# Optimization experiments

Hardware: AMD Instinct MI355X
Metric: run time of the kernel (lower is better)

The kernel has to match this reference:

```python
import jax, jax.numpy as jnp
import numpy as np

N, E, B = 65536, 131072, 2048
NUM_FEATURES, EDGE_FEATURES, DIM = 75, 16, 64


def setup_inputs() -> dict:
    key = jax.random.key(0)
    ks = jax.random.split(key, 24)

    def p(i, shape, scale=0.05):
        return jax.random.normal(ks[i], shape, dtype=jnp.float32) * scale

    return {
        "node_features": p(0, (N, NUM_FEATURES), 1.0),
        "edge_features": p(1, (E, EDGE_FEATURES), 1.0),
        "edge_index": jax.random.randint(ks[2], (2, E), 0, N),
        "graph_index": jnp.sort(jax.random.randint(ks[3], (N,), 0, B)),
        "lin0_w": p(4, (NUM_FEATURES, DIM)),
        "lin0_b": p(5, (DIM,)),
        "mlp_w1": p(6, (EDGE_FEATURES, 128)),
        "mlp_b1": p(7, (128,)),
        "mlp_w2": p(8, (128, DIM * DIM)),
        "mlp_b2": p(9, (DIM * DIM,)),
        "conv_bias": p(10, (DIM,)),
        "gru_w_ih": p(11, (3 * DIM, DIM)),
        "gru_w_hh": p(12, (3 * DIM, DIM)),
        "gru_b_ih": p(13, (3 * DIM,)),
        "gru_b_hh": p(14, (3 * DIM,)),
        "lstm_w_ih": p(15, (4 * DIM, 2 * DIM)),
        "lstm_w_hh": p(16, (4 * DIM, DIM)),
        "lstm_b_ih": p(17, (4 * DIM,)),
        "lstm_b_hh": p(18, (4 * DIM,)),
    }


def reference(node_features, edge_features, edge_index, graph_index,
              lin0_w, lin0_b, mlp_w1, mlp_b1, mlp_w2, mlp_b2, conv_bias,
              gru_w_ih, gru_w_hh, gru_b_ih, gru_b_hh,
              lstm_w_ih, lstm_w_hh, lstm_b_ih, lstm_b_hh):
    n = node_features.shape[0]
    d = DIM
    src, dst = edge_index[0], edge_index[1]

    # edge-conditioned weights (identical every iteration in the original loop)
    ew = jnp.maximum(edge_features @ mlp_w1 + mlp_b1, 0.0) @ mlp_w2 + mlp_b2
    W = ew.reshape(-1, d, d)  # [E, d, d]
    counts = jnp.maximum(
        jax.ops.segment_sum(jnp.ones(src.shape[0], jnp.float32), dst, num_segments=n), 1.0)

    out = jnp.maximum(node_features @ lin0_w + lin0_b, 0.0)
    h = out
    for _ in range(3):
        # NNConv: gather src, per-edge matmul, scatter-mean to dst
        msg = jnp.einsum('ed,edf->ef', out[src], W)
        agg = jax.ops.segment_sum(msg, dst, num_segments=n) / counts[:, None]
        m = jnp.maximum(agg + conv_bias, 0.0)
        # GRU step (seq len 1)
        gi = m @ gru_w_ih.T + gru_b_ih
        gh = h @ gru_w_hh.T + gru_b_hh
        r = jax.nn.sigmoid(gi[:, :d] + gh[:, :d])
        z = jax.nn.sigmoid(gi[:, d:2 * d] + gh[:, d:2 * d])
        nn_ = jnp.tanh(gi[:, 2 * d:] + r * gh[:, 2 * d:])
        h = (1.0 - z) * nn_ + z * h
        out = h
    feat_map = out

    # Set2Set pooling, 3 processing steps
    q_star = jnp.zeros((B, 2 * d), jnp.float32)
    hs = jnp.zeros((B, d), jnp.float32)
    cs = jnp.zeros((B, d), jnp.float32)
    for _ in range(3):
        gates = q_star @ lstm_w_ih.T + lstm_b_ih + hs @ lstm_w_hh.T + lstm_b_hh
        i_g = jax.nn.sigmoid(gates[:, :d])
        f_g = jax.nn.sigmoid(gates[:, d:2 * d])
        g_g = jnp.tanh(gates[:, 2 * d:3 * d])
        o_g = jax.nn.sigmoid(gates[:, 3 * d:])
        cs = f_g * cs + i_g * g_g
        hs = o_g * jnp.tanh(cs)
        q = hs  # [B, d]
        e = jnp.sum(out * q[graph_index], axis=-1)  # [N]
        e = e - jax.ops.segment_max(e, graph_index, num_segments=B)[graph_index]
        a = jnp.exp(e)
        a = a / (jax.ops.segment_sum(a, graph_index, num_segments=B)[graph_index] + 1e-16)
        rvec = jax.ops.segment_sum(a[:, None] * out, graph_index, num_segments=B)
        q_star = jnp.concatenate([q, rvec], axis=-1)
    return (q_star, feat_map)
```

## Files before the change

kernel.cpp:

```cpp
#include <hip/hip_runtime.h>
#include <hip/hip_bf16.h>

#define GN 65536
#define GE 131072
#define GB 2048

typedef __attribute__((ext_vector_type(8))) short short8;
typedef __attribute__((ext_vector_type(4))) float floatx4;

static __device__ __forceinline__ float sigm(float x) { return 1.0f / (1.0f + __expf(-x)); }
static __device__ __forceinline__ float bf2f(unsigned short u) {
    union { unsigned int i; float f; } v; v.i = ((unsigned int)u) << 16; return v.f;
}
static __device__ __forceinline__ int geti(const void* p, long long i, int f64) {
    return f64 ? (int)((const long long*)p)[i] : ((const int*)p)[i];
}

struct DetectArgs { const void* src[17]; int nhalf[17]; int fi[17]; };
__global__ void k_detect(DetectArgs a, const unsigned int* __restrict__ pe,
                         const unsigned int* __restrict__ pg,
                         int* __restrict__ flags, int* __restrict__ flagE,
                         int* __restrict__ flagG) {
    __shared__ unsigned int sA[256], sB[256];
    if (blockIdx.x >= 17) {
        const unsigned int* p = (blockIdx.x == 17) ? pe : pg;
        const long long nwords = (blockIdx.x == 17) ? (long long)2 * GE : (long long)GN;
        const long long lim = nwords < 16384 ? nwords : 16384;
        unsigned int acc = 0;
        for (long long w = 1 + 2 * (long long)threadIdx.x; w < lim; w += 512) acc |= p[w];
        sA[threadIdx.x] = acc;
        __syncthreads();
        for (int st = 128; st > 0; st >>= 1) {
            if (threadIdx.x < st) sA[threadIdx.x] |= sA[threadIdx.x + st];
            __syncthreads();
        }
        if (threadIdx.x == 0) *((blockIdx.x == 17) ? flagE : flagG) = (sA[0] == 0u) ? 1 : 0;
        return;
    }
    const unsigned short* p = (const unsigned short*)a.src[blockIdx.x];
    const int n0 = a.nhalf[blockIdx.x];
    const int n = n0 < 16384 ? n0 : 16384;
    unsigned int any = 0, orEven = 0;
    for (int i = threadIdx.x; i < n; i += 256) {
        const unsigned short u = p[i];
        const float av = fabsf(bf2f(u));
        if (!(av <= 1e6f)) any = 1u;
        if ((i & 1) == 0) orEven |= u;
    }
    sA[threadIdx.x] = any; sB[threadIdx.x] = orEven;
    __syncthreads();
    for (int s = 128; s > 0; s >>= 1) {
        if (threadIdx.x < s) {
            sA[threadIdx.x] |= sA[threadIdx.x + s];
            sB[threadIdx.x] |= sB[threadIdx.x + s];
        }
        __syncthreads();
    }
    if (threadIdx.x == 0) flags[a.fi[blockIdx.x]] = (sA[0] || sB[0] == 0u) ? 1 : 0;
}

struct CvtArgs { const void* src[15]; float* dst[15]; int n[15]; int fi[15]; int pre[16]; };
__global__ void k_cvt_all(CvtArgs a, const int* __restrict__ flags) {
    const int b = blockIdx.x;
    int t = 0;
    while (t < 14 && b >= a.pre[t + 1]) ++t;
    const int i = (b - a.pre[t]) * 256 + threadIdx.x;
    if (i >= a.n[t]) return;
    const int f = flags[a.fi[t]];
    a.dst[t][i] = f ? ((const float*)a.src[t])[i] : bf2f(((const unsigned short*)a.src[t])[i]);
}

__global__ __launch_bounds__(256) void k_t2(const void* __restrict__ src,
                                            __hip_bfloat16* __restrict__ w2P,
                                            const int* __restrict__ flag) {
    const int tid8 = blockIdx.x * 256 + threadIdx.x;
    const int quad = tid8 & 3, lr = (tid8 >> 2) & 15, rb = (tid8 >> 6) & 7,
              kk = (tid8 >> 9) & 3, t = tid8 >> 11;
    const int n = t * 128 + rb * 16 + lr;
    const int k0 = kk * 32 + quad * 8;
    const int isf32 = *flag;
    short8 v;
    #pragma unroll
    for (int j = 0; j < 8; ++j) {
        const size_t si = (size_t)(k0 + j) * 4096 + n;
        const float f = isf32 ? ((const float*)src)[si] : bf2f(((const unsigned short*)src)[si]);
        const __hip_bfloat16 b = __float2bfloat16(f);
        v[j] = *(const short*)&b;
    }
    *(short8*)(w2P + (size_t)tid8 * 8) = v;
}

__global__ void k_gpack2(const float* __restrict__ w_ih, const float* __restrict__ w_hh,
                         __hip_bfloat16* __restrict__ gwp) {
    const int t = blockIdx.x * 256 + threadIdx.x;
    if (t >= 3072) return;
    const int lane = t & 63;
    const int kk = (t >> 6) & 1;
    const int nb = (t >> 7) % 12;
    const int mat = t / 1536;
    const float* W = mat ? w_hh : w_ih;
    const int c = nb * 16 + (lane & 15);
    const int k0 = kk * 32 + (lane >> 4) * 8;
    short8 hi, lo;
    #pragma unroll
    for (int j = 0; j < 8; ++j) {
        const float v = W[c * 64 + k0 + j];
        const __hip_bfloat16 bh = __float2bfloat16(v);
        hi[j] = *(const short*)&bh;
        const __hip_bfloat16 bl = __float2bfloat16(v - __bfloat162float(bh));
        lo[j] = *(const short*)&bl;
    }
    const size_t base = (size_t)(((mat * 12 + nb) * 2 + kk) * 2);
    *(short8*)(gwp + (base + 0) * 512 + lane * 8) = hi;
    *(short8*)(gwp + (base + 1) * 512 + lane * 8) = lo;
}

__global__ void k_counts(const void* __restrict__ eidx, const int* __restrict__ fi64,
                         float* __restrict__ counts, int E_) {
    int e = blockIdx.x * 256 + threadIdx.x;
    if (e < E_) atomicAdd(&counts[geti(eidx, (long long)E_ + e, *fi64)], 1.0f);
}

__global__ void k_rowptr(const void* __restrict__ gi, const int* __restrict__ fi64,
                         int* __restrict__ rowptr, int N_, int B_) {
    int g = blockIdx.x * 256 + threadIdx.x;
    if (g > B_) return;
    const int f64 = *fi64;
    int lo = 0, hi = N_;
    while (lo < hi) { int mid = (lo + hi) >> 1; if (geti(gi, mid, f64) < g) lo = mid + 1; else hi = mid; }
    rowptr[g] = lo;
}

__global__ __launch_bounds__(256) void k_lin0(const void* __restrict__ nf_raw,
                                              const float* __restrict__ w,
                                              const float* __restrict__ b,
                                              float* __restrict__ out,
                                              const int* __restrict__ flag) {
    const int ln = threadIdx.x >> 6;
    const int d = threadIdx.x & 63;
    const int n = blockIdx.x * 4 + ln;
    const int isf32 = *flag;
    __shared__ float s_nf[4][76];
    const size_t base = (size_t)n * 75;
    s_nf[ln][d] = isf32 ? ((const float*)nf_raw)[base + d] : bf2f(((const unsigned short*)nf_raw)[base + d]);
    if (d < 11) s_nf[ln][64 + d] = isf32 ? ((const float*)nf_raw)[base + 64 + d]
                                         : bf2f(((const unsigned short*)nf_raw)[base + 64 + d]);
    __syncthreads();
    float acc = b[d];
    #pragma unroll
    for (int i = 0; i < 75; ++i) acc += s_nf[ln][i] * w[i * 64 + d];
    out[(size_t)n * 64 + d] = fmaxf(acc, 0.0f);
}

__global__ __launch_bounds__(256) void k1_h1(const void* __restrict__ ef_raw,
                                             const float* __restrict__ w1,
                                             const float* __restrict__ b1,
                                             __hip_bfloat16* __restrict__ h1,
                                             const int* __restrict__ flag) {
    const int le = threadIdx.x >> 7;
    const int j = threadIdx.x & 127;
    const int e = blockIdx.x * 2 + le;
    const int isf32 = *flag;
    __shared__ float efs[2][16];
    if (j < 16) {
        const size_t idx = (size_t)e * 16 + j;
        efs[le][j] = isf32 ? ((const float*)ef_raw)[idx] : bf2f(((const unsigned short*)ef_raw)[idx]);
    }
    __syncthreads();
    float acc = b1[j];
    #pragma unroll
    for (int i = 0; i < 16; ++i) acc += efs[le][i] * w1[i * 128 + j];
    h1[(size_t)e * 128 + j] = __float2bfloat16(fmaxf(acc, 0.0f));
}

__global__ __launch_bounds__(512) void k23_fused(const __hip_bfloat16* __restrict__ h1,
                                                 const __hip_bfloat16* __restrict__ w2P,
                                                 const float* __restrict__ b2,
                                                 const float* __restrict__ out,
                                                 const void* __restrict__ eidx,
                                                 const int* __restrict__ fi64,
                                                 float* __restrict__ agg) {
    __shared__ __align__(16) __hip_bfloat16 As[128 * 128];
    __shared__ float yT[64][65];
    const int tid = threadIdx.x;
    const int e0 = blockIdx.x * 128;
    const int f64 = *fi64;

    const int wave = tid >> 6, lane = tid & 63;
    const int wm = (wave >> 2) * 64;
    const int wn = (wave & 3) * 32;
    const int lr = lane & 15, quad = lane >> 4;

    {
        const int r = tid >> 2;
        const int cb = (tid & 3) * 32;
        #pragma unroll
        for (int j = 0; j < 4; ++j) {
            const int c = cb + j * 8;
            short8 v = *(const short8*)(h1 + (size_t)(e0 + r) * 128 + c);
            const int byte = (r * 256 + c * 2) ^ ((r & 7) << 4);
            *(short8*)((char*)As + byte) = v;
        }
    }
    __shared__ float yT2[64][129];
    {
        const int e = tid >> 2, d0 = (tid & 3) * 16;
        const int s = geti(eidx, e0 + e, f64);
        const float* srow = out + (size_t)s * 64 + d0;
        #pragma unroll
        for (int j = 0; j < 4; ++j) {
            float4 v = *(const float4*)(srow + j * 4);
            yT2[d0 + j * 4 + 0][e] = v.x;
            yT2[d0 + j * 4 + 1][e] = v.y;
            yT2[d0 + j * 4 + 2][e] = v.z;
            yT2[d0 + j * 4 + 3][e] = v.w;
        }
    }
    __syncthreads();

    const int lin = (lr * 4 + quad) * 8;
    const int sxa = (lr & 7) << 4;
    float msum[4][2][4] = {};

#define K23_LOADB(dst, tt)                                                      \
    _Pragma("unroll")                                                           \
    for (int kk = 0; kk < 4; ++kk) {                                            \
        _Pragma("unroll")                                                       \
        for (int nt = 0; nt < 2; ++nt) {                                        \
            const int g = ((tt) * 4 + kk) * 8 + (wn >> 4) + nt;                 \
            dst[kk][nt] = *(const short8*)(w2P + (size_t)g * 512 + lin);        \
        }                                                                       \
    }                                                                           \
    __builtin_amdgcn_sched_barrier(0);

#define K23_BODY(tt, buf) {                                                     \
    const int n0 = (tt) * 128;                                                  \
    const int dcur = (n0 + wn) >> 6;                                            \
    const float b2v0 = b2[n0 + wn + lr];                                        \
    const float b2v1 = b2[n0 + wn + 16 + lr];                                   \
    floatx4 acc[4][2] = {};                                                     \
    _Pragma("unroll")                                                           \
    for (int kk = 0; kk < 4; ++kk) {                                            \
        short8 a0, a1, a2, a3;                                                  \
        {                                                                       \
            const int cb = kk * 64 + quad * 16;                                 \
            a0 = *(const short8*)((const char*)As + (((wm + 0 * 16 + lr) * 256 + cb) ^ sxa)); \
            a1 = *(const short8*)((const char*)As + (((wm + 1 * 16 + lr) * 256 + cb) ^ sxa)); \
            a2 = *(const short8*)((const char*)As + (((wm + 2 * 16 + lr) * 256 + cb) ^ sxa)); \
            a3 = *(const short8*)((const char*)As + (((wm + 3 * 16 + lr) * 256 + cb) ^ sxa)); \
        }                                                                       \
        __builtin_amdgcn_s_setprio(1);                                          \
        acc[0][0] = __builtin_amdgcn_mfma_f32_16x16x32_bf16(a0, buf[kk][0], acc[0][0], 0, 0, 0); \
        acc[0][1] = __builtin_amdgcn_mfma_f32_16x16x32_bf16(a0, buf[kk][1], acc[0][1], 0, 0, 0); \
        acc[1][0] = __builtin_amdgcn_mfma_f32_16x16x32_bf16(a1, buf[kk][0], acc[1][0], 0, 0, 0); \
        acc[1][1] = __builtin_amdgcn_mfma_f32_16x16x32_bf16(a1, buf[kk][1], acc[1][1], 0, 0, 0); \
        acc[2][0] = __builtin_amdgcn_mfma_f32_16x16x32_bf16(a2, buf[kk][0], acc[2][0], 0, 0, 0); \
        acc[2][1] = __builtin_amdgcn_mfma_f32_16x16x32_bf16(a2, buf[kk][1], acc[2][1], 0, 0, 0); \
        acc[3][0] = __builtin_amdgcn_mfma_f32_16x16x32_bf16(a3, buf[kk][0], acc[3][0], 0, 0, 0); \
        acc[3][1] = __builtin_amdgcn_mfma_f32_16x16x32_bf16(a3, buf[kk][1], acc[3][1], 0, 0, 0); \
        __builtin_amdgcn_s_setprio(0);                                          \
    }                                                                           \
    _Pragma("unroll")                                                           \
    for (int mt = 0; mt < 4; ++mt) {                                            \
        _Pragma("unroll")                                                       \
        for (int r = 0; r < 4; ++r) {                                           \
            const float yv = yT2[dcur][wm + mt * 16 + quad * 4 + r];            \
            msum[mt][0][r] = fmaf(yv, acc[mt][0][r] + b2v0, msum[mt][0][r]);    \
            msum[mt][1][r] = fmaf(yv, acc[mt][1][r] + b2v1, msum[mt][1][r]);    \
        }                                                                       \
    }                                                                           \
}

    short8 bA[4][2], bB[4][2];
    K23_LOADB(bA, 0)
    #pragma unroll 1
    for (int t = 0; t < 32; t += 2) {
        K23_LOADB(bB, t + 1)
        K23_BODY(t, bA)
        if (t + 2 < 32) { K23_LOADB(bA, t + 2) }
        K23_BODY(t + 1, bB)
    }
#undef K23_LOADB
#undef K23_BODY

    const int fbase = (wn & 32);
    #pragma unroll
    for (int mt = 0; mt < 4; ++mt)
        #pragma unroll
        for (int r = 0; r < 4; ++r) {
            const int row = wm + mt * 16 + quad * 4 + r;
            const int dn = geti(eidx, (long long)GE + e0 + row, f64);
            #pragma unroll
            for (int nt = 0; nt < 2; ++nt)
                atomicAdd(&agg[(size_t)dn * 64 + fbase + nt * 16 + lr], msum[mt][nt][r]);
        }
}

__global__ __launch_bounds__(256) void k4_gru(const float* __restrict__ agg,
                                              const float* __restrict__ counts,
                                              const float* __restrict__ cbias,
                                              const __hip_bfloat16* __restrict__ gwp,
                                              const float* __restrict__ b_ih,
                                              const float* __restrict__ b_hh,
                                              float* __restrict__ out) {
    const int wv = threadIdx.x >> 6, lane = threadIdx.x & 63;
    const int lr = lane & 15, quad = lane >> 4;
    const int wnb0 = blockIdx.x * 64 + wv * 16;
    const int node = wnb0 + lr;

    const float rcnt = 1.0f / fmaxf(counts[node], 1.0f);
    const float* ap = agg + (size_t)node * 64;
    const float* hp = out + (size_t)node * 64;
    short8 am[2], ah[2];
    #pragma unroll
    for (int kk = 0; kk < 2; ++kk) {
        const int k0 = kk * 32 + quad * 8;
        #pragma unroll
        for (int j = 0; j < 8; ++j) {
            const float mv = fmaxf(ap[k0 + j] * rcnt + cbias[k0 + j], 0.0f);
            const __hip_bfloat16 mb = __float2bfloat16(mv);
            am[kk][j] = *(const short*)&mb;
            const __hip_bfloat16 hb = __float2bfloat16(hp[k0 + j]);
            ah[kk][j] = *(const short*)&hb;
        }
    }

    floatx4 ai[12] = {}, ahh[12] = {};
    #pragma unroll
    for (int nb = 0; nb < 12; ++nb) {
        #pragma unroll
        for (int kk = 0; kk < 2; ++kk) {
            #pragma unroll
            for (int part = 0; part < 2; ++part) {
                const short8 bi = *(const short8*)(gwp + (size_t)(((0 * 12 + nb) * 2 + kk) * 2 + part) * 512 + lane * 8);
                ai[nb] = __builtin_amdgcn_mfma_f32_16x16x32_bf16(am[kk], bi, ai[nb], 0, 0, 0);
                const short8 bh = *(const short8*)(gwp + (size_t)(((1 * 12 + nb) * 2 + kk) * 2 + part) * 512 + lane * 8);
                ahh[nb] = __builtin_amdgcn_mfma_f32_16x16x32_bf16(ah[kk], bh, ahh[nb], 0, 0, 0);
            }
        }
    }

    #pragma unroll
    for (int f = 0; f < 4; ++f) {
        const int d = f * 16 + lr;
        const float bir = b_ih[d],       bhr = b_hh[d];
        const float biz = b_ih[64 + d],  bhz = b_hh[64 + d];
        const float bin = b_ih[128 + d], bhn = b_hh[128 + d];
        #pragma unroll
        for (int r = 0; r < 4; ++r) {
            const int row = wnb0 + quad * 4 + r;
            const float rr = sigm(ai[f][r] + bir + ahh[f][r] + bhr);
            const float zz = sigm(ai[f + 4][r] + biz + ahh[f + 4][r] + bhz);
            const float nn = tanhf(ai[f + 8][r] + bin + rr * (ahh[f + 8][r] + bhn));
            const float hd = out[(size_t)row * 64 + d];
            out[(size_t)row * 64 + d] = (1.0f - zz) * nn + zz * hd;
        }
    }
}

__global__ __launch_bounds__(256) void k5_fused(float* __restrict__ qstar,
                                                const float* __restrict__ w_ih,
                                                const float* __restrict__ w_hh,
                                                const float* __restrict__ b_ih,
                                                const float* __restrict__ b_hh,
                                                const float* __restrict__ out,
                                                const int* __restrict__ rowptr) {
    const int g = blockIdx.x;
    const int j = threadIdx.x;
    __shared__ float qs[128], hv[64], gates[256];
    __shared__ float smw[4], sSw[4], srw[4][64];
    if (j < 128) qs[j] = 0.0f;
    if (j < 64) hv[j] = 0.0f;
    float creg = 0.0f;
    const int wv = j >> 6, lane = j & 63;
    const int start = rowptr[g], end = rowptr[g + 1];
    const float bsum = b_ih[j] + b_hh[j];

    for (int step = 0; step < 3; ++step) {
        __syncthreads();
        float acc = bsum;
        for (int k4 = 0; k4 < 128; k4 += 4) {
            float4 v = *(const float4*)(w_ih + (size_t)j * 128 + k4);
            const float* pv = (const float*)&v;
            #pragma unroll
            for (int t = 0; t < 4; ++t) acc += qs[k4 + t] * pv[t];
        }
        for (int k4 = 0; k4 < 64; k4 += 4) {
            float4 v = *(const float4*)(w_hh + (size_t)j * 64 + k4);
            const float* pv = (const float*)&v;
            #pragma unroll
            for (int t = 0; t < 4; ++t) acc += hv[k4 + t] * pv[t];
        }
        gates[j] = acc;
        __syncthreads();
        if (j < 64) {
            const float ig = sigm(gates[j]);
            const float fg = sigm(gates[64 + j]);
            const float gg = tanhf(gates[128 + j]);
            const float og = sigm(gates[192 + j]);
            creg = fg * creg + ig * gg;
            const float h = og * tanhf(creg);
            hv[j] = h;
            qs[j] = h;
        }
        __syncthreads();
        const float q = hv[lane];
        float m = -3.4e38f, S = 0.0f, racc = 0.0f;
        for (int n = start + wv; n < end; n += 4) {
            const float ov = out[(size_t)n * 64 + lane];
            float p = ov * q;
            #pragma unroll
            for (int off = 1; off < 64; off <<= 1) p += __shfl_xor(p, off);
            if (p > m) {
                const float sc = __expf(m - p);
                S = S * sc + 1.0f;
                racc = racc * sc + ov;
                m = p;
            } else {
                const float w = __expf(p - m);
                S += w;
                racc += w * ov;
            }
        }
        if (lane == 0) { smw[wv] = m; sSw[wv] = S; }
        srw[wv][lane] = racc;
        __syncthreads();
        if (wv == 0) {
            const float mstar = fmaxf(fmaxf(smw[0], smw[1]), fmaxf(smw[2], smw[3]));
            float Ssum = 0.0f, rsum = 0.0f;
            #pragma unroll
            for (int i = 0; i < 4; ++i) {
                const float sc = __expf(smw[i] - mstar);
                Ssum += sSw[i] * sc;
                rsum += srw[i][lane] * sc;
            }
            qs[64 + lane] = rsum / (Ssum + 1e-16f);
        }
    }
    __syncthreads();
    if (j < 128) qstar[(size_t)g * 128 + j] = qs[j];
}

__global__ void k_out(const float* __restrict__ qstar, const float* __restrict__ outb,
                      float* __restrict__ dst, int nq, int nfeat, int out_n) {
    int i = blockIdx.x * 256 + threadIdx.x;
    if (i >= out_n) return;
    float v = 0.0f;
    if (i < nq) v = qstar[i];
    else if (i - nq < nfeat) v = outb[i - nq];
    dst[i] = v;
}

extern "C" void kernel_launch(void* const* d_in, const int* in_sizes, int n_in,
                              void* d_out, int out_size, void* d_ws, size_t ws_size,
                              hipStream_t stream) {
    constexpr int N = GN, E = GE, B = GB;

    char* ws = (char*)d_ws;
    size_t off = 0;
    auto alloc = [&](size_t bytes) { size_t o = off; off = (off + bytes + 255) & ~(size_t)255; return o; };

    int*   fl     = (int*)  (ws + alloc(19 * 4));
    int*   flagE  = (int*)  (ws + alloc(256));
    int*   flagG  = (int*)  (ws + alloc(256));
    float* counts = (float*)(ws + alloc((size_t)N * 4));
    int*   rowptr = (int*)  (ws + alloc((size_t)(B + 1) * 4));
    float* outbuf = (float*)(ws + alloc((size_t)N * 64 * 4));
    float* agg    = (float*)(ws + alloc((size_t)N * 64 * 4));
    float* qstar  = (float*)(ws + alloc((size_t)B * 128 * 4));
    __hip_bfloat16* h1  = (__hip_bfloat16*)(ws + alloc((size_t)E * 128 * 2));
    __hip_bfloat16* w2P = (__hip_bfloat16*)(ws + alloc((size_t)4096 * 128 * 2));
    __hip_bfloat16* gwp = (__hip_bfloat16*)(ws + alloc((size_t)2 * 12 * 2 * 2 * 512 * 2));

    const int fidx[15]  = {4, 5, 6, 7, 8, 9, 10, 11, 12, 13, 14, 15, 16, 17, 18};
    const int fsize[15] = {75 * 64, 64, 16 * 128, 128, 128 * 4096, 4096, 64,
                           192 * 64, 192 * 64, 192, 192, 256 * 128, 256 * 64, 256, 256};
    float* F[19] = {};
    for (int t = 0; t < 15; ++t) F[fidx[t]] = (float*)(ws + alloc((size_t)fsize[t] * 4));

    DetectArgs da;
    da.src[0] = d_in[0]; da.nhalf[0] = N * 75; da.fi[0] = 0;
    da.src[1] = d_in[1]; da.nhalf[1] = E * 16; da.fi[1] = 1;
    for (int t = 0; t < 15; ++t) { da.src[2 + t] = d_in[fidx[t]]; da.nhalf[2 + t] = fsize[t]; da.fi[2 + t] = fidx[t]; }
    k_detect<<<19, 256, 0, stream>>>(da, (const unsigned int*)d_in[2],
                                     (const unsigned int*)d_in[3], fl, flagE, flagG);

    CvtArgs ca;
    int pre = 0;
    for (int t = 0; t < 15; ++t) {
        ca.src[t] = d_in[fidx[t]]; ca.dst[t] = F[fidx[t]]; ca.n[t] = fsize[t]; ca.fi[t] = fidx[t];
        ca.pre[t] = pre; pre += (fsize[t] + 255) / 256;
    }
    ca.pre[15] = pre;
    k_cvt_all<<<pre, 256, 0, stream>>>(ca, fl);
    k_t2<<<256, 256, 0, stream>>>(d_in[8], w2P, fl + 8);
    k_gpack2<<<12, 256, 0, stream>>>(F[11], F[12], gwp);

    hipMemsetAsync(counts, 0, (size_t)N * 4, stream);
    hipMemsetAsync(qstar, 0, (size_t)B * 128 * 4, stream);

    k_counts<<<E / 256, 256, 0, stream>>>(d_in[2], flagE, counts, E);
    k_rowptr<<<(B + 1 + 255) / 256, 256, 0, stream>>>(d_in[3], flagG, rowptr, N, B);
    k_lin0<<<N / 4, 256, 0, stream>>>(d_in[0], F[4], F[5], outbuf, fl + 0);
    k1_h1<<<E / 2, 256, 0, stream>>>(d_in[1], F[6], F[7], h1, fl + 1);

    for (int it = 0; it < 3; ++it) {
        hipMemsetAsync(agg, 0, (size_t)N * 64 * 4, stream);
        k23_fused<<<E / 128, 512, 0, stream>>>(h1, w2P, F[9], outbuf, d_in[2], flagE, agg);
        k4_gru<<<N / 64, 256, 0, stream>>>(agg, counts, F[10], gwp, F[13], F[14], outbuf);
    }
    k5_fused<<<B, 256, 0, stream>>>(qstar, F[15], F[16], F[17], F[18], outbuf, rowptr);
    k_out<<<(out_size + 255) / 256, 256, 0, stream>>>(qstar, outbuf, (float*)d_out,
                                                      B * 128, N * 64, out_size);
}
```

Measured before the change: 1.053 ms.

## Shrink edge tile to 64 and reduce partial messages in LDS before atomics

The fused edge-weight/message kernel now handles 64 edges per 256-thread block instead of 128 edges per 512 threads. All four waves share the same A rows and split the output columns. Waves whose column slices map to the same feature half first sum their partials in shared memory. The block then issues one coalesced atomicAdd per (edge, feature), using destination indices cached in LDS. This halves global atomic traffic and lowers LDS use so more blocks can be resident, but each block now re-reads the full w2 weight matrix for half as many edges and adds extra barriers.

```diff
diff --git a/kernel.cpp b/kernel.cpp
--- a/kernel.cpp
+++ b/kernel.cpp
@@ -173,24 +173,25 @@
     h1[(size_t)e * 128 + j] = __float2bfloat16(fmaxf(acc, 0.0f));
 }
 
-__global__ __launch_bounds__(512) void k23_fused(const __hip_bfloat16* __restrict__ h1,
+__global__ __launch_bounds__(256) void k23_fused(const __hip_bfloat16* __restrict__ h1,
                                                  const __hip_bfloat16* __restrict__ w2P,
                                                  const float* __restrict__ b2,
                                                  const float* __restrict__ out,
                                                  const void* __restrict__ eidx,
                                                  const int* __restrict__ fi64,
                                                  float* __restrict__ agg) {
-    __shared__ __align__(16) __hip_bfloat16 As[128 * 128];
+    __shared__ __align__(16) __hip_bfloat16 As[64 * 128];
     __shared__ float yT[64][65];
+    __shared__ int sdx[64];
     const int tid = threadIdx.x;
-    const int e0 = blockIdx.x * 128;
+    const int e0 = blockIdx.x * 64;
     const int f64 = *fi64;
 
     const int wave = tid >> 6, lane = tid & 63;
-    const int wm = (wave >> 2) * 64;
-    const int wn = (wave & 3) * 32;
+    const int wn = wave * 32;
     const int lr = lane & 15, quad = lane >> 4;
 
+    if (tid < 64) sdx[tid] = geti(eidx, (long long)GE + e0 + tid, f64);
     {
         const int r = tid >> 2;
         const int cb = (tid & 3) * 32;
@@ -202,7 +203,6 @@
             *(short8*)((char*)As + byte) = v;
         }
     }
-    __shared__ float yT2[64][129];
     {
         const int e = tid >> 2, d0 = (tid & 3) * 16;
         const int s = geti(eidx, e0 + e, f64);
@@ -210,10 +210,10 @@
         #pragma unroll
         for (int j = 0; j < 4; ++j) {
             float4 v = *(const float4*)(srow + j * 4);
-            yT2[d0 + j * 4 + 0][e] = v.x;
-            yT2[d0 + j * 4 + 1][e] = v.y;
-            yT2[d0 + j * 4 + 2][e] = v.z;
-            yT2[d0 + j * 4 + 3][e] = v.w;
+            yT[d0 + j * 4 + 0][e] = v.x;
+            yT[d0 + j * 4 + 1][e] = v.y;
+            yT[d0 + j * 4 + 2][e] = v.z;
+            yT[d0 + j * 4 + 3][e] = v.w;
         }
     }
     __syncthreads();
@@ -244,10 +244,10 @@
         short8 a0, a1, a2, a3;                                                  \
         {                                                                       \
             const int cb = kk * 64 + quad * 16;                                 \
-            a0 = *(const short8*)((const char*)As + (((wm + 0 * 16 + lr) * 256 + cb) ^ sxa)); \
-            a1 = *(const short8*)((const char*)As + (((wm + 1 * 16 + lr) * 256 + cb) ^ sxa)); \
-            a2 = *(const short8*)((const char*)As + (((wm + 2 * 16 + lr) * 256 + cb) ^ sxa)); \
-            a3 = *(const short8*)((const char*)As + (((wm + 3 * 16 + lr) * 256 + cb) ^ sxa)); \
+            a0 = *(const short8*)((const char*)As + (((0 * 16 + lr) * 256 + cb) ^ sxa)); \
+            a1 = *(const short8*)((const char*)As + (((1 * 16 + lr) * 256 + cb) ^ sxa)); \
+            a2 = *(const short8*)((const char*)As + (((2 * 16 + lr) * 256 + cb) ^ sxa)); \
+            a3 = *(const short8*)((const char*)As + (((3 * 16 + lr) * 256 + cb) ^ sxa)); \
         }                                                                       \
         __builtin_amdgcn_s_setprio(1);                                          \
         acc[0][0] = __builtin_amdgcn_mfma_f32_16x16x32_bf16(a0, buf[kk][0], acc[0][0], 0, 0, 0); \
@@ -264,7 +264,7 @@
     for (int mt = 0; mt < 4; ++mt) {                                            \
         _Pragma("unroll")                                                       \
         for (int r = 0; r < 4; ++r) {                                           \
-            const float yv = yT2[dcur][wm + mt * 16 + quad * 4 + r];            \
+            const float yv = yT[dcur][mt * 16 + quad * 4 + r];                  \
             msum[mt][0][r] = fmaf(yv, acc[mt][0][r] + b2v0, msum[mt][0][r]);    \
             msum[mt][1][r] = fmaf(yv, acc[mt][1][r] + b2v1, msum[mt][1][r]);    \
         }                                                                       \
@@ -283,17 +283,35 @@
 #undef K23_LOADB
 #undef K23_BODY
 
-    const int fbase = (wn & 32);
-    #pragma unroll
-    for (int mt = 0; mt < 4; ++mt)
-        #pragma unroll
-        for (int r = 0; r < 4; ++r) {
-            const int row = wm + mt * 16 + quad * 4 + r;
-            const int dn = geti(eidx, (long long)GE + e0 + row, f64);
-            #pragma unroll
-            for (int nt = 0; nt < 2; ++nt)
-                atomicAdd(&agg[(size_t)dn * 64 + fbase + nt * 16 + lr], msum[mt][nt][r]);
-        }
+    __syncthreads();
+    float* mg = (float*)As;
+    const int fb = (wn & 32);
+    if (wave < 2) {
+        #pragma unroll
+        for (int mt = 0; mt < 4; ++mt)
+            #pragma unroll
+            for (int r = 0; r < 4; ++r)
+                #pragma unroll
+                for (int nt = 0; nt < 2; ++nt)
+                    mg[(mt * 16 + quad * 4 + r) * 64 + fb + nt * 16 + lr] = msum[mt][nt][r];
+    }
+    __syncthreads();
+    if (wave >= 2) {
+        #pragma unroll
+        for (int mt = 0; mt < 4; ++mt)
+            #pragma unroll
+            for (int r = 0; r < 4; ++r)
+                #pragma unroll
+                for (int nt = 0; nt < 2; ++nt)
+                    mg[(mt * 16 + quad * 4 + r) * 64 + fb + nt * 16 + lr] += msum[mt][nt][r];
+    }
+    __syncthreads();
+    #pragma unroll
+    for (int i = 0; i < 16; ++i) {
+        const int o = i * 256 + tid;
+        const int row = o >> 6, col = o & 63;
+        atomicAdd(&agg[(size_t)sdx[row] * 64 + col], mg[o]);
+    }
 }
 
 __global__ __launch_bounds__(256) void k4_gru(const float* __restrict__ agg,
@@ -506,7 +524,7 @@
 
     for (int it = 0; it < 3; ++it) {
         hipMemsetAsync(agg, 0, (size_t)N * 64 * 4, stream);
-        k23_fused<<<E / 128, 512, 0, stream>>>(h1, w2P, F[9], outbuf, d_in[2], flagE, agg);
+        k23_fused<<<E / 64, 256, 0, stream>>>(h1, w2P, F[9], outbuf, d_in[2], flagE, agg);
         k4_gru<<<N / 64, 256, 0, stream>>>(agg, counts, F[10], gwp, F[13], F[14], outbuf);
     }
     k5_fused<<<B, 256, 0, stream>>>(qstar, F[15], F[16], F[17], F[18], outbuf, rowptr);
```

Result: faster. 972.6 us (-7.7%).
